# Kernel optimization log

Hardware: AMD Instinct MI355X
Metric: run time of the kernel (lower is better)

## Reference

```python
import jax, jax.numpy as jnp
import numpy as np

K_NEIGHBOURS = 4  # neighbour_num
BN_EPS = 1e-5


def setup_inputs() -> dict:
    key = jax.random.key(0)
    ks = jax.random.split(key, 5)
    B, T, J, C = 32, 243, 17, 256
    std = np.sqrt(2.0 / C).astype(np.float32)
    return {
        "x": jax.random.normal(ks[0], (B, T, J, C), dtype=jnp.float32),
        "W_u": jax.random.normal(ks[1], (C, C), dtype=jnp.float32) * std,
        "b_u": jnp.zeros((C,), dtype=jnp.float32),
        "W_v": jax.random.normal(ks[2], (C, C), dtype=jnp.float32) * std,
        "b_v": jnp.zeros((C,), dtype=jnp.float32),
        "gamma": jnp.ones((T,), dtype=jnp.float32),
        "beta": jnp.zeros((T,), dtype=jnp.float32),
    }


def reference(x, W_u, b_u, W_v, b_v, gamma, beta):
    # temporal-mode GCN with top-k similarity adjacency
    b, t, j, c = x.shape
    xr = jnp.transpose(x, (0, 2, 1, 3)).reshape(b * j, t, c)  # [BJ, T, C]

    # similarity adjacency: keep edges >= k-th largest similarity per row
    sim = jnp.einsum('bnc,bmc->bnm', xr, xr)                  # [BJ, T, T]
    thr = jax.lax.top_k(sim, K_NEIGHBOURS)[0][..., -1:]       # [BJ, T, 1]
    adj = (sim >= thr).astype(x.dtype)

    # symmetric degree normalization D^{-1/2} A D^{-1/2}
    deg_inv_sqrt = adj.sum(-1) ** -0.5                        # [BJ, T]
    norm_adj = deg_inv_sqrt[:, :, None] * adj * deg_inv_sqrt[:, None, :]

    v = xr @ W_v.T + b_v
    u = xr @ W_u.T + b_u
    h = jnp.einsum('bnm,bmc->bnc', norm_adj, v) + u           # [BJ, T, C]

    # BatchNorm1d(num_features=T), training mode: stats over (batch, C)
    mean = h.mean(axis=(0, 2), keepdims=True)
    var = jnp.mean((h - mean) ** 2, axis=(0, 2), keepdims=True)
    hn = (h - mean) * jax.lax.rsqrt(var + BN_EPS) * gamma[None, :, None] + beta[None, :, None]

    out = jax.nn.relu(xr + hn)                                # residual (dim_in == dim_out)
    return jnp.transpose(out.reshape(b, j, t, c), (0, 2, 1, 3))  # [B, T, J, C]
```

## Files before the change

kernel.cpp:

```cpp
#include <hip/hip_runtime.h>

#define BB 32
#define TT 243
#define JJ 17
#define CC 256
#define BJC (BB*JJ)
#define MM (BJC*TT)
#define FR (BJC*256)
#define SIMP 244
#define NEG_INF (-3.0e38f)

typedef __attribute__((ext_vector_type(8))) short bf16x8;
typedef __attribute__((ext_vector_type(4))) float f32x4;
typedef __attribute__((ext_vector_type(8))) _Float16 f16x8;
typedef __attribute__((ext_vector_type(4))) _Float16 f16x4;

__device__ __forceinline__ unsigned short f2bf(float f) {
  unsigned int u = __float_as_uint(f);
  u = (u + 0x7fffu + ((u >> 16) & 1u)) >> 16;
  return (unsigned short)u;
}
__device__ __forceinline__ float bf2f(unsigned short s) {
  return __uint_as_float(((unsigned int)s) << 16);
}

__device__ __forceinline__ void gld16(const void* g, void* l) {
  __builtin_amdgcn_global_load_lds(
      (__attribute__((address_space(1))) void*)(g),
      (__attribute__((address_space(3))) void*)(l), 16, 0, 0);
}

__launch_bounds__(256)
__global__ void k_prep_w(const float* __restrict__ Wu, const float* __restrict__ Wv,
                         _Float16* __restrict__ wcp) {
  const int r = blockIdx.x * 4 + (threadIdx.x >> 6);
  const int l = threadIdx.x & 63;
  const float* src = ((r < CC) ? (Wu + (size_t)r * CC) : (Wv + (size_t)(r - CC) * CC)) + l * 4;
  float4 v = *reinterpret_cast<const float4*>(src);
  f16x4 hv = (f16x4){(_Float16)v.x, (_Float16)v.y, (_Float16)v.z, (_Float16)v.w};
  const int ks = l >> 4;
  const int u  = (l & 15) >> 1;
  const int s  = u ^ (r & 7);
  *reinterpret_cast<f16x4*>(wcp + ((size_t)ks * 512 + r) * 64 + s * 8 + (l & 1) * 4) = hv;
}

__launch_bounds__(256)
__global__ void k_prep_x(const float* __restrict__ x,
                         _Float16* __restrict__ xqh, _Float16* __restrict__ xql) {
  const int r = blockIdx.x * 4 + (threadIdx.x >> 6);
  const int l = threadIdx.x & 63;
  const int bj = r / TT, t = r - bj * TT;
  const int b = bj / JJ, j = bj - b * JJ;
  float4 v = *reinterpret_cast<const float4*>(
      x + ((size_t)(b * TT + t) * JJ + j) * CC + l * 4);
  _Float16 h0 = (_Float16)v.x, h1 = (_Float16)v.y, h2 = (_Float16)v.z, h3 = (_Float16)v.w;
  f16x4 hv = (f16x4){h0, h1, h2, h3};
  f16x4 lv = (f16x4){(_Float16)(v.x - (float)h0), (_Float16)(v.y - (float)h1),
                     (_Float16)(v.z - (float)h2), (_Float16)(v.w - (float)h3)};
  const int fr = bj * 256 + t;
  const int ks = l >> 4;
  const int u  = (l & 15) >> 1;
  const int s  = u ^ (t & 7);
  const size_t off = ((size_t)ks * FR + fr) * 64 + s * 8 + (l & 1) * 4;
  *reinterpret_cast<f16x4*>(xqh + off) = hv;
  *reinterpret_cast<f16x4*>(xql + off) = lv;
}

__launch_bounds__(512, 4)
__global__ void k_sim(const _Float16* __restrict__ xqh, const _Float16* __restrict__ xql,
                      float* __restrict__ sim) {
  __shared__ _Float16 Sh[256 * 64];
  __shared__ _Float16 Sl[256 * 64];
  const int bid = blockIdx.x;
  const int g = bid >> 4, s_ = bid & 15;
  const int bj = g * 8 + (s_ & 7);
  const int rh = s_ >> 3;
  const int tid = threadIdx.x, lane = tid & 63, wid = tid >> 6;
  const int wr = wid >> 2, wc = wid & 3;
  const int rowbase = rh * 128 + wr * 64;
  const int l15 = lane & 15, lg = lane >> 4;
  const size_t rb = (size_t)bj * 256;
  const size_t lsrc = (size_t)(lane >> 3) * 64 + (lane & 7) * 8;

  f32x4 acc[4][4];
  #pragma unroll
  for (int i = 0; i < 4; i++)
    #pragma unroll
    for (int j = 0; j < 4; j++) acc[i][j] = (f32x4){0.f, 0.f, 0.f, 0.f};

  for (int ks = 0; ks < 4; ++ks) {
    {
      const _Float16* ph = xqh + ((size_t)ks * FR + rb) * 64;
      const _Float16* pl = xql + ((size_t)ks * FR + rb) * 64;
      #pragma unroll
      for (int c = 0; c < 4; ++c) {
        const int row0 = (wid * 4 + c) * 8;
        gld16(ph + (size_t)row0 * 64 + lsrc, &Sh[row0 * 64]);
        gld16(pl + (size_t)row0 * 64 + lsrc, &Sl[row0 * 64]);
      }
    }
    __syncthreads();
    #pragma unroll
    for (int kh = 0; kh < 2; ++kh) {
      f16x8 bhv[4], blv[4];
      #pragma unroll
      for (int j = 0; j < 4; ++j) {
        int rc = wc * 64 + j * 16 + l15;
        int sl = ((kh * 4 + lg) ^ (rc & 7)) * 8;
        bhv[j] = *reinterpret_cast<const f16x8*>(&Sh[rc * 64 + sl]);
        blv[j] = *reinterpret_cast<const f16x8*>(&Sl[rc * 64 + sl]);
      }
      #pragma unroll
      for (int i = 0; i < 4; ++i) {
        int rl = rowbase + i * 16 + l15;
        int sl = ((kh * 4 + lg) ^ (rl & 7)) * 8;
        f16x8 ah = *reinterpret_cast<const f16x8*>(&Sh[rl * 64 + sl]);
        f16x8 al = *reinterpret_cast<const f16x8*>(&Sl[rl * 64 + sl]);
        #pragma unroll
        for (int j = 0; j < 4; ++j) {
          acc[i][j] = __builtin_amdgcn_mfma_f32_16x16x32_f16(ah, bhv[j], acc[i][j], 0, 0, 0);
          acc[i][j] = __builtin_amdgcn_mfma_f32_16x16x32_f16(ah, blv[j], acc[i][j], 0, 0, 0);
          acc[i][j] = __builtin_amdgcn_mfma_f32_16x16x32_f16(al, bhv[j], acc[i][j], 0, 0, 0);
        }
      }
    }
    if (ks < 3) __syncthreads();
  }

  const size_t sbase = (size_t)bj * TT * SIMP;
  #pragma unroll
  for (int i = 0; i < 4; ++i) {
    #pragma unroll
    for (int q = 0; q < 4; ++q) {
      int n = rowbase + i * 16 + lg * 4 + q;
      if (n < TT) {
        #pragma unroll
        for (int j = 0; j < 4; ++j) {
          int c = wc * 64 + j * 16 + l15;
          if (c < TT) sim[sbase + (size_t)n * SIMP + c] = acc[i][j][q];
        }
      }
    }
  }
}

__launch_bounds__(256)
__global__ void k_uv(const _Float16* __restrict__ xqh, const _Float16* __restrict__ wcp,
                     const float* __restrict__ bu, const float* __restrict__ bv,
                     unsigned short* __restrict__ uo, unsigned short* __restrict__ vo) {
  __shared__ _Float16 S[2][128][64];
  const int ct = blockIdx.x;
  const int m0 = blockIdx.y * 128;
  const int tid = threadIdx.x, lane = tid & 63, wid = tid >> 6;
  const int rm = wid * 32;
  const int l15 = lane & 15, lg = lane >> 4;

  const float* bsrc = (ct < 2) ? bu : bv;
  unsigned short* osrc = (ct < 2) ? uo : vo;
  const int cb = (ct & 1) * 128;

  float bias[8];
  #pragma unroll
  for (int j = 0; j < 8; ++j) bias[j] = bsrc[cb + j * 16 + l15];

  f32x4 acc[2][8];
  #pragma unroll
  for (int i = 0; i < 2; i++)
    #pragma unroll
    for (int j = 0; j < 8; j++) acc[i][j] = (f32x4){0.f, 0.f, 0.f, 0.f};

  for (int ks = 0; ks < 4; ++ks) {
    #pragma unroll
    for (int c = 0; c < 8; ++c) {
      int ch = wid * 8 + c;
      int half = ch >> 4;
      int rows0 = (ch & 15) * 8;
      const _Float16* g = half
        ? wcp + ((size_t)ks * 512 + ct * 128 + rows0) * 64 + lane * 8
        : xqh + ((size_t)ks * FR  + m0       + rows0) * 64 + lane * 8;
      gld16(g, &S[half][rows0][0]);
    }
    __syncthreads();
    #pragma unroll
    for (int kh = 0; kh < 2; ++kh) {
      f16x8 af[2], bfv[8];
      #pragma unroll
      for (int i = 0; i < 2; ++i) {
        int rl = rm + i * 16 + l15;
        af[i] = *reinterpret_cast<const f16x8*>(&S[0][rl][((kh * 4 + lg) ^ (rl & 7)) * 8]);
      }
      #pragma unroll
      for (int j = 0; j < 8; ++j) {
        int rl = j * 16 + l15;
        bfv[j] = *reinterpret_cast<const f16x8*>(&S[1][rl][((kh * 4 + lg) ^ (rl & 7)) * 8]);
      }
      #pragma unroll
      for (int i = 0; i < 2; ++i)
        #pragma unroll
        for (int j = 0; j < 8; ++j)
          acc[i][j] = __builtin_amdgcn_mfma_f32_16x16x32_f16(af[i], bfv[j], acc[i][j], 0, 0, 0);
    }
    __syncthreads();
  }

  #pragma unroll
  for (int i = 0; i < 2; ++i) {
    #pragma unroll
    for (int q = 0; q < 4; ++q) {
      int gf = m0 + rm + i * 16 + lg * 4 + q;
      int t = gf & 255, bj = gf >> 8;
      if (t < TT) {
        size_t gm = (size_t)bj * TT + t;
        #pragma unroll
        for (int j = 0; j < 8; ++j)
          osrc[gm * CC + cb + j * 16 + l15] = f2bf(acc[i][j][q] + bias[j]);
      }
    }
  }
}

__launch_bounds__(256)
__global__ void k_topk(const float* __restrict__ sim,
                       float* __restrict__ dis_o,
                       unsigned long long* __restrict__ mask_o,
                       unsigned char* __restrict__ nbr_o,
                       unsigned char* __restrict__ deg_o) {
  const int l = threadIdx.x & 63, wv = threadIdx.x >> 6;
  const int r = blockIdx.x * 4 + wv;
  const float* row = sim + (size_t)r * SIMP;
  float o0 = row[l];
  float o1 = row[l + 64];
  float o2 = row[l + 128];
  float o3 = (l + 192 < TT) ? row[l + 192] : NEG_INF;
  float v0 = o0, v1 = o1, v2 = o2, v3 = o3;
  { float mx, mn;
    mx=fmaxf(v0,v1); mn=fminf(v0,v1); v0=mx; v1=mn;
    mx=fmaxf(v2,v3); mn=fminf(v2,v3); v2=mx; v3=mn;
    mx=fmaxf(v0,v2); mn=fminf(v0,v2); v0=mx; v2=mn;
    mx=fmaxf(v1,v3); mn=fminf(v1,v3); v1=mx; v3=mn;
    mx=fmaxf(v1,v2); mn=fminf(v1,v2); v1=mx; v2=mn; }
  #pragma unroll
  for (int off = 1; off < 64; off <<= 1) {
    float b0 = __shfl_xor(v0, off), b1 = __shfl_xor(v1, off),
          b2 = __shfl_xor(v2, off), b3 = __shfl_xor(v3, off);
    float t0 = fmaxf(v0, b3), t1 = fmaxf(v1, b2),
          t2 = fmaxf(v2, b1), t3 = fmaxf(v3, b0);
    float mx, mn;
    mx=fmaxf(t0,t2); mn=fminf(t0,t2); t0=mx; t2=mn;
    mx=fmaxf(t1,t3); mn=fminf(t1,t3); t1=mx; t3=mn;
    mx=fmaxf(t0,t1); mn=fminf(t0,t1); t0=mx; t1=mn;
    mx=fmaxf(t2,t3); mn=fminf(t2,t3); t2=mx; t3=mn;
    v0=t0; v1=t1; v2=t2; v3=t3;
  }
  const float thr = v3;

  unsigned long long m0 = __ballot(o0 >= thr);
  unsigned long long m1 = __ballot(o1 >= thr);
  unsigned long long m2 = __ballot(o2 >= thr);
  unsigned long long m3 = __ballot(o3 >= thr);
  const unsigned long long below = (1ull << l) - 1ull;
  const int b0 = __popcll(m0);
  const int b1 = b0 + __popcll(m1);
  const int b2 = b1 + __popcll(m2);
  const size_t r8 = (size_t)r * 8;
  if (o0 >= thr) { int q = __popcll(m0 & below);      if (q < 8) nbr_o[r8 + q] = (unsigned char)l; }
  if (o1 >= thr) { int q = b0 + __popcll(m1 & below); if (q < 8) nbr_o[r8 + q] = (unsigned char)(64 + l); }
  if (o2 >= thr) { int q = b1 + __popcll(m2 & below); if (q < 8) nbr_o[r8 + q] = (unsigned char)(128 + l); }
  if (o3 >= thr) { int q = b2 + __popcll(m3 & below); if (q < 8) nbr_o[r8 + q] = (unsigned char)(192 + l); }
  if (l == 0) {
    int deg = b2 + __popcll(m3);
    dis_o[r] = rsqrtf((float)deg);
    deg_o[r] = (unsigned char)((deg > 255) ? 255 : deg);
    mask_o[(size_t)r * 4 + 0] = m0;
    mask_o[(size_t)r * 4 + 1] = m1;
    mask_o[(size_t)r * 4 + 2] = m2;
    mask_o[(size_t)r * 4 + 3] = m3;
  }
}

__launch_bounds__(512)
__global__ void k_agg(const unsigned char* __restrict__ nbr,
                      const unsigned char* __restrict__ degv,
                      const unsigned long long* __restrict__ mask,
                      const float* __restrict__ dis,
                      const unsigned short* __restrict__ u,
                      const unsigned short* __restrict__ v,
                      unsigned short* __restrict__ h,
                      float* __restrict__ p1, float* __restrict__ p2) {
  __shared__ float dis_l[256];
  const int bj = blockIdx.x;
  const int tid = threadIdx.x, lane = tid & 63, wid = tid >> 6;
  if (tid < TT) dis_l[tid] = dis[(size_t)bj * TT + tid];
  __syncthreads();
  const int start = blockIdx.y * 122;
  const int cnt = blockIdx.y ? (TT - 122) : 122;
  const size_t pbase = (size_t)bj * TT;
  const int co = lane * 4;
  for (int rl = wid; rl < cnt; rl += 8) {
    const int t = start + rl;
    const size_t r = pbase + t;
    const float dr = dis_l[t];
    const int dg = degv[r];
    const unsigned long long nb = *reinterpret_cast<const unsigned long long*>(nbr + r * 8);
    ushort4 uu = *reinterpret_cast<const ushort4*>(u + r * CC + co);
    float a0 = bf2f(uu.x), a1 = bf2f(uu.y), a2 = bf2f(uu.z), a3 = bf2f(uu.w);
    if (dg <= 8) {
      const int i0 = (int)(nb & 255), i1 = (int)((nb >> 8) & 255),
                i2 = (int)((nb >> 16) & 255), i3 = (int)((nb >> 24) & 255);
      ushort4 w0v = *reinterpret_cast<const ushort4*>(v + (pbase + i0) * CC + co);
      ushort4 w1v = *reinterpret_cast<const ushort4*>(v + (pbase + i1) * CC + co);
      ushort4 w2v = *reinterpret_cast<const ushort4*>(v + (pbase + i2) * CC + co);
      ushort4 w3v = *reinterpret_cast<const ushort4*>(v + (pbase + i3) * CC + co);
      const float w0 = dr * dis_l[i0], w1 = dr * dis_l[i1],
                  w2 = dr * dis_l[i2], w3 = dr * dis_l[i3];
      a0 = __builtin_fmaf(w0, bf2f(w0v.x), a0); a1 = __builtin_fmaf(w0, bf2f(w0v.y), a1);
      a2 = __builtin_fmaf(w0, bf2f(w0v.z), a2); a3 = __builtin_fmaf(w0, bf2f(w0v.w), a3);
      a0 = __builtin_fmaf(w1, bf2f(w1v.x), a0); a1 = __builtin_fmaf(w1, bf2f(w1v.y), a1);
      a2 = __builtin_fmaf(w1, bf2f(w1v.z), a2); a3 = __builtin_fmaf(w1, bf2f(w1v.w), a3);
      a0 = __builtin_fmaf(w2, bf2f(w2v.x), a0); a1 = __builtin_fmaf(w2, bf2f(w2v.y), a1);
      a2 = __builtin_fmaf(w2, bf2f(w2v.z), a2); a3 = __builtin_fmaf(w2, bf2f(w2v.w), a3);
      a0 = __builtin_fmaf(w3, bf2f(w3v.x), a0); a1 = __builtin_fmaf(w3, bf2f(w3v.y), a1);
      a2 = __builtin_fmaf(w3, bf2f(w3v.z), a2); a3 = __builtin_fmaf(w3, bf2f(w3v.w), a3);
      #pragma unroll
      for (int e = 4; e < 8; ++e) {
        if (e < dg) {
          const int ix = (int)((nb >> (8 * e)) & 255);
          const float we = dr * dis_l[ix];
          ushort4 vv = *reinterpret_cast<const ushort4*>(v + (pbase + ix) * CC + co);
          a0 = __builtin_fmaf(we, bf2f(vv.x), a0); a1 = __builtin_fmaf(we, bf2f(vv.y), a1);
          a2 = __builtin_fmaf(we, bf2f(vv.z), a2); a3 = __builtin_fmaf(we, bf2f(vv.w), a3);
        }
      }
    } else {
      #pragma unroll
      for (int w4 = 0; w4 < 4; ++w4) {
        unsigned long long m = mask[r * 4 + w4];
        while (m) {
          int i = __ffsll(m) - 1;
          m &= m - 1;
          int idx = w4 * 64 + i;
          float w = dr * dis_l[idx];
          ushort4 vv = *reinterpret_cast<const ushort4*>(v + (pbase + idx) * CC + co);
          a0 = __builtin_fmaf(w, bf2f(vv.x), a0);
          a1 = __builtin_fmaf(w, bf2f(vv.y), a1);
          a2 = __builtin_fmaf(w, bf2f(vv.z), a2);
          a3 = __builtin_fmaf(w, bf2f(vv.w), a3);
        }
      }
    }
    ushort4 hh;
    hh.x = f2bf(a0); hh.y = f2bf(a1); hh.z = f2bf(a2); hh.w = f2bf(a3);
    *reinterpret_cast<ushort4*>(h + r * CC + co) = hh;
    float s1 = a0 + a1 + a2 + a3;
    float s2 = a0*a0 + a1*a1 + a2*a2 + a3*a3;
    #pragma unroll
    for (int off = 1; off < 64; off <<= 1) { s1 += __shfl_xor(s1, off); s2 += __shfl_xor(s2, off); }
    if (lane == 0) { p1[r] = s1; p2[r] = s2; }
  }
}

__global__ void k_bnstat(const float* __restrict__ p1, const float* __restrict__ p2,
                         const float* __restrict__ gamma, const float* __restrict__ beta,
                         float* __restrict__ scale, float* __restrict__ shift) {
  __shared__ float sA[256], sB[256];
  const int t = blockIdx.x;
  const int tid = threadIdx.x;
  float a = 0.f, b2 = 0.f;
  for (int bj = tid; bj < BJC; bj += 256) {
    a  += p1[bj * TT + t];
    b2 += p2[bj * TT + t];
  }
  sA[tid] = a; sB[tid] = b2;
  __syncthreads();
  for (int s = 128; s > 0; s >>= 1) {
    if (tid < s) { sA[tid] += sA[tid + s]; sB[tid] += sB[tid + s]; }
    __syncthreads();
  }
  if (tid == 0) {
    const float invN = 1.0f / (float)(BJC * CC);
    float mean = sA[0] * invN;
    float var  = sB[0] * invN - mean * mean;
    float sc   = rsqrtf(var + 1e-5f) * gamma[t];
    scale[t] = sc;
    shift[t] = beta[t] - mean * sc;
  }
}

__global__ void k_out(const float* __restrict__ x, const unsigned short* __restrict__ h,
                      const float* __restrict__ scale, const float* __restrict__ shift,
                      float* __restrict__ out) {
  int g = blockIdx.x * 256 + threadIdx.x;
  if (g >= MM * (CC/4)) return;
  int c4  = g & 63;
  int rowx = g >> 6;
  int b   = rowx / (TT*JJ);
  int rem = rowx - b*(TT*JJ);
  int t   = rem / JJ;
  int j   = rem - t*JJ;
  size_t hoff = ((size_t)(b*JJ + j) * TT + t) * CC + c4*4;
  float4 xv = *reinterpret_cast<const float4*>(x + (size_t)rowx*CC + c4*4);
  ushort4 hv = *reinterpret_cast<const ushort4*>(h + hoff);
  float sc = scale[t], sh = shift[t];
  float4 o;
  o.x = fmaxf(xv.x + bf2f(hv.x)*sc + sh, 0.f);
  o.y = fmaxf(xv.y + bf2f(hv.y)*sc + sh, 0.f);
  o.z = fmaxf(xv.z + bf2f(hv.z)*sc + sh, 0.f);
  o.w = fmaxf(xv.w + bf2f(hv.w)*sc + sh, 0.f);
  *reinterpret_cast<float4*>(out + (size_t)rowx*CC + c4*4) = o;
}

extern "C" void kernel_launch(void* const* d_in, const int* in_sizes, int n_in,
                              void* d_out, int out_size, void* d_ws, size_t ws_size,
                              hipStream_t stream) {
  const float* x     = (const float*)d_in[0];
  const float* Wu    = (const float*)d_in[1];
  const float* bu    = (const float*)d_in[2];
  const float* Wv    = (const float*)d_in[3];
  const float* bv    = (const float*)d_in[4];
  const float* gamma = (const float*)d_in[5];
  const float* beta  = (const float*)d_in[6];
  float* out = (float*)d_out;

  char* ws = (char*)d_ws;
  size_t off = 0;
  auto alloc = [&](size_t bytes) -> void* {
    void* p = ws + off;
    off = (off + bytes + 255) & ~(size_t)255;
    return p;
  };
  _Float16* xqh = (_Float16*)alloc((size_t)4 * FR * 64 * 2);
  _Float16* xql = (_Float16*)alloc((size_t)4 * FR * 64 * 2);
  _Float16* wcp = (_Float16*)alloc((size_t)4 * 512 * 64 * 2);
  float* sim = (float*)alloc((size_t)BJC * TT * SIMP * 4);
  float* dis = (float*)alloc((size_t)MM * 4);
  unsigned long long* msk = (unsigned long long*)alloc((size_t)MM * 4 * 8);
  unsigned char* nbr = (unsigned char*)alloc((size_t)MM * 8);
  unsigned char* deg = (unsigned char*)alloc((size_t)MM);
  float* p1    = (float*)alloc((size_t)MM * 4);
  float* p2    = (float*)alloc((size_t)MM * 4);
  float* scale = (float*)alloc(1024);
  float* shift = (float*)alloc(1024);
  unsigned short* v = (unsigned short*)alloc((size_t)MM * CC * 2);
  unsigned short* u = (unsigned short*)sim;
  unsigned short* h = (unsigned short*)xql;

  if (ws_size < off) {
    hipMemsetAsync(d_out, 0, (size_t)out_size * 4, stream);
    return;
  }

  k_prep_w<<<dim3(512/4), dim3(256), 0, stream>>>(Wu, Wv, wcp);
  k_prep_x<<<dim3(MM/4), dim3(256), 0, stream>>>(x, xqh, xql);
  k_sim  <<<dim3(BJC*2), dim3(512), 0, stream>>>(xqh, xql, sim);
  k_topk <<<dim3(MM/4), dim3(256), 0, stream>>>(sim, dis, msk, nbr, deg);
  k_uv   <<<dim3(4, FR/128), dim3(256), 0, stream>>>(xqh, wcp, bu, bv, u, v);
  k_agg  <<<dim3(BJC, 2), dim3(512), 0, stream>>>(nbr, deg, msk, dis, u, v, h, p1, p2);
  k_bnstat<<<dim3(TT), dim3(256), 0, stream>>>(p1, p2, gamma, beta, scale, shift);
  k_out  <<<dim3((MM*(CC/4) + 255)/256), dim3(256), 0, stream>>>(x, h, scale, shift, out);
}
```

Before: 385.5 us.

## Fuse top-k threshold selection into similarity GEMM epilogue, drop sim buffer

```diff
diff --git a/kernel.cpp b/kernel.cpp
--- a/kernel.cpp
+++ b/kernel.cpp
@@ -7,7 +7,6 @@
 #define BJC (BB*JJ)
 #define MM (BJC*TT)
 #define FR (BJC*256)
-#define SIMP 244
 #define NEG_INF (-3.0e38f)
 
 typedef __attribute__((ext_vector_type(8))) short bf16x8;
@@ -68,9 +67,13 @@
 
 __launch_bounds__(512, 4)
 __global__ void k_sim(const _Float16* __restrict__ xqh, const _Float16* __restrict__ xql,
-                      float* __restrict__ sim) {
-  __shared__ _Float16 Sh[256 * 64];
-  __shared__ _Float16 Sl[256 * 64];
+                      float* __restrict__ dis_o,
+                      unsigned long long* __restrict__ mask_o,
+                      unsigned char* __restrict__ nbr_o,
+                      unsigned char* __restrict__ deg_o) {
+  __shared__ __align__(16) char LB[65536];
+  _Float16* Sh = (_Float16*)LB;
+  _Float16* Sl = (_Float16*)(LB + 32768);
   const int bid = blockIdx.x;
   const int g = bid >> 4, s_ = bid & 15;
   const int bj = g * 8 + (s_ & 7);
@@ -95,8 +98,8 @@
       #pragma unroll
       for (int c = 0; c < 4; ++c) {
         const int row0 = (wid * 4 + c) * 8;
-        gld16(ph + (size_t)row0 * 64 + lsrc, &Sh[row0 * 64]);
-        gld16(pl + (size_t)row0 * 64 + lsrc, &Sl[row0 * 64]);
+        gld16(ph + (size_t)row0 * 64 + lsrc, Sh + row0 * 64);
+        gld16(pl + (size_t)row0 * 64 + lsrc, Sl + row0 * 64);
       }
     }
     __syncthreads();
@@ -124,22 +127,118 @@
         }
       }
     }
-    if (ks < 3) __syncthreads();
-  }
-
-  const size_t sbase = (size_t)bj * TT * SIMP;
+    __syncthreads();
+  }
+
+  float* top4 = (float*)LB;
+  unsigned long long* mlds = (unsigned long long*)(LB + 8192);
+  float* thrl = (float*)(LB + 8192 + 4096);
+
+  auto mval = [&](int i, int j, int q) -> float {
+    float x = acc[i][j][q];
+    if (wc == 3 && j == 3 && l15 >= 3) x = NEG_INF;
+    return x;
+  };
+
   #pragma unroll
   for (int i = 0; i < 4; ++i) {
     #pragma unroll
     for (int q = 0; q < 4; ++q) {
-      int n = rowbase + i * 16 + lg * 4 + q;
-      if (n < TT) {
+      float v0 = mval(i, 0, q), v1 = mval(i, 1, q),
+            v2 = mval(i, 2, q), v3 = mval(i, 3, q);
+      { float mx, mn;
+        mx=fmaxf(v0,v1); mn=fminf(v0,v1); v0=mx; v1=mn;
+        mx=fmaxf(v2,v3); mn=fminf(v2,v3); v2=mx; v3=mn;
+        mx=fmaxf(v0,v2); mn=fminf(v0,v2); v0=mx; v2=mn;
+        mx=fmaxf(v1,v3); mn=fminf(v1,v3); v1=mx; v3=mn;
+        mx=fmaxf(v1,v2); mn=fminf(v1,v2); v1=mx; v2=mn; }
+      #pragma unroll
+      for (int off = 1; off < 16; off <<= 1) {
+        float b0 = __shfl_xor(v0, off), b1 = __shfl_xor(v1, off),
+              b2 = __shfl_xor(v2, off), b3 = __shfl_xor(v3, off);
+        float t0 = fmaxf(v0, b3), t1 = fmaxf(v1, b2),
+              t2 = fmaxf(v2, b1), t3 = fmaxf(v3, b0);
+        float mx, mn;
+        mx=fmaxf(t0,t2); mn=fminf(t0,t2); t0=mx; t2=mn;
+        mx=fmaxf(t1,t3); mn=fminf(t1,t3); t1=mx; t3=mn;
+        mx=fmaxf(t0,t1); mn=fminf(t0,t1); t0=mx; t1=mn;
+        mx=fmaxf(t2,t3); mn=fminf(t2,t3); t2=mx; t3=mn;
+        v0=t0; v1=t1; v2=t2; v3=t3;
+      }
+      if (l15 == 0) {
+        int rloc = wr * 64 + i * 16 + lg * 4 + q;
+        float* d = &top4[(rloc * 4 + wc) * 4];
+        d[0] = v0; d[1] = v1; d[2] = v2; d[3] = v3;
+      }
+    }
+  }
+  __syncthreads();
+
+  if (tid < 128) {
+    float t0 = NEG_INF, t1 = NEG_INF, t2 = NEG_INF, t3 = NEG_INF;
+    #pragma unroll
+    for (int w = 0; w < 4; ++w) {
+      #pragma unroll
+      for (int e = 0; e < 4; ++e) {
+        float xv = top4[(tid * 4 + w) * 4 + e];
+        if (xv > t3) {
+          if (xv > t0)      { t3 = t2; t2 = t1; t1 = t0; t0 = xv; }
+          else if (xv > t1) { t3 = t2; t2 = t1; t1 = xv; }
+          else if (xv > t2) { t3 = t2; t2 = xv; }
+          else              { t3 = xv; }
+        }
+      }
+    }
+    thrl[tid] = t3;
+  }
+  __syncthreads();
+
+  #pragma unroll
+  for (int i = 0; i < 4; ++i) {
+    #pragma unroll
+    for (int q = 0; q < 4; ++q) {
+      const int rloc = wr * 64 + i * 16 + lg * 4 + q;
+      const float th = thrl[rloc];
+      unsigned long long bal[4];
+      #pragma unroll
+      for (int j = 0; j < 4; ++j) bal[j] = __ballot(mval(i, j, q) >= th);
+      if (l15 == 0) {
+        unsigned long long m = 0;
         #pragma unroll
-        for (int j = 0; j < 4; ++j) {
-          int c = wc * 64 + j * 16 + l15;
-          if (c < TT) sim[sbase + (size_t)n * SIMP + c] = acc[i][j][q];
+        for (int j = 0; j < 4; ++j)
+          m |= ((bal[j] >> (lg * 16)) & 0xFFFFull) << (j * 16);
+        mlds[rloc * 4 + wc] = m;
+      }
+    }
+  }
+  __syncthreads();
+
+  if (tid < 128) {
+    const int rn = rh * 128 + tid;
+    if (rn < TT) {
+      const size_t r = (size_t)bj * TT + rn;
+      unsigned long long m0 = mlds[tid * 4 + 0], m1 = mlds[tid * 4 + 1],
+                         m2 = mlds[tid * 4 + 2], m3 = mlds[tid * 4 + 3];
+      int deg = __popcll(m0) + __popcll(m1) + __popcll(m2) + __popcll(m3);
+      dis_o[r] = rsqrtf((float)deg);
+      deg_o[r] = (unsigned char)((deg > 255) ? 255 : deg);
+      mask_o[r * 4 + 0] = m0;
+      mask_o[r * 4 + 1] = m1;
+      mask_o[r * 4 + 2] = m2;
+      mask_o[r * 4 + 3] = m3;
+      unsigned long long nbv = 0;
+      int cnt = 0;
+      #pragma unroll
+      for (int w4 = 0; w4 < 4; ++w4) {
+        unsigned long long m = (w4 == 0) ? m0 : (w4 == 1) ? m1 : (w4 == 2) ? m2 : m3;
+        while (m && cnt < 8) {
+          int b = __ffsll(m) - 1;
+          m &= m - 1;
+          nbv |= ((unsigned long long)(w4 * 64 + b)) << (8 * cnt);
+          ++cnt;
         }
       }
+      *reinterpret_cast<unsigned long long*>(nbr_o + r * 8) = nbv;
     }
   }
 }
@@ -216,65 +315,6 @@
           osrc[gm * CC + cb + j * 16 + l15] = f2bf(acc[i][j][q] + bias[j]);
       }
     }
-  }
-}
-
-__launch_bounds__(256)
-__global__ void k_topk(const float* __restrict__ sim,
-                       float* __restrict__ dis_o,
-                       unsigned long long* __restrict__ mask_o,
-                       unsigned char* __restrict__ nbr_o,
-                       unsigned char* __restrict__ deg_o) {
-  const int l = threadIdx.x & 63, wv = threadIdx.x >> 6;
-  const int r = blockIdx.x * 4 + wv;
-  const float* row = sim + (size_t)r * SIMP;
-  float o0 = row[l];
-  float o1 = row[l + 64];
-  float o2 = row[l + 128];
-  float o3 = (l + 192 < TT) ? row[l + 192] : NEG_INF;
-  float v0 = o0, v1 = o1, v2 = o2, v3 = o3;
-  { float mx, mn;
-    mx=fmaxf(v0,v1); mn=fminf(v0,v1); v0=mx; v1=mn;
-    mx=fmaxf(v2,v3); mn=fminf(v2,v3); v2=mx; v3=mn;
-    mx=fmaxf(v0,v2); mn=fminf(v0,v2); v0=mx; v2=mn;
-    mx=fmaxf(v1,v3); mn=fminf(v1,v3); v1=mx; v3=mn;
-    mx=fmaxf(v1,v2); mn=fminf(v1,v2); v1=mx; v2=mn; }
-  #pragma unroll
-  for (int off = 1; off < 64; off <<= 1) {
-    float b0 = __shfl_xor(v0, off), b1 = __shfl_xor(v1, off),
-          b2 = __shfl_xor(v2, off), b3 = __shfl_xor(v3, off);
-    float t0 = fmaxf(v0, b3), t1 = fmaxf(v1, b2),
-          t2 = fmaxf(v2, b1), t3 = fmaxf(v3, b0);
-    float mx, mn;
-    mx=fmaxf(t0,t2); mn=fminf(t0,t2); t0=mx; t2=mn;
-    mx=fmaxf(t1,t3); mn=fminf(t1,t3); t1=mx; t3=mn;
-    mx=fmaxf(t0,t1); mn=fminf(t0,t1); t0=mx; t1=mn;
-    mx=fmaxf(t2,t3); mn=fminf(t2,t3); t2=mx; t3=mn;
-    v0=t0; v1=t1; v2=t2; v3=t3;
-  }
-  const float thr = v3;
-
-  unsigned long long m0 = __ballot(o0 >= thr);
-  unsigned long long m1 = __ballot(o1 >= thr);
-  unsigned long long m2 = __ballot(o2 >= thr);
-  unsigned long long m3 = __ballot(o3 >= thr);
-  const unsigned long long below = (1ull << l) - 1ull;
-  const int b0 = __popcll(m0);
-  const int b1 = b0 + __popcll(m1);
-  const int b2 = b1 + __popcll(m2);
-  const size_t r8 = (size_t)r * 8;
-  if (o0 >= thr) { int q = __popcll(m0 & below);      if (q < 8) nbr_o[r8 + q] = (unsigned char)l; }
-  if (o1 >= thr) { int q = b0 + __popcll(m1 & below); if (q < 8) nbr_o[r8 + q] = (unsigned char)(64 + l); }
-  if (o2 >= thr) { int q = b1 + __popcll(m2 & below); if (q < 8) nbr_o[r8 + q] = (unsigned char)(128 + l); }
-  if (o3 >= thr) { int q = b2 + __popcll(m3 & below); if (q < 8) nbr_o[r8 + q] = (unsigned char)(192 + l); }
-  if (l == 0) {
-    int deg = b2 + __popcll(m3);
-    dis_o[r] = rsqrtf((float)deg);
-    deg_o[r] = (unsigned char)((deg > 255) ? 255 : deg);
-    mask_o[(size_t)r * 4 + 0] = m0;
-    mask_o[(size_t)r * 4 + 1] = m1;
-    mask_o[(size_t)r * 4 + 2] = m2;
-    mask_o[(size_t)r * 4 + 3] = m3;
   }
 }
 
@@ -431,7 +471,6 @@
   _Float16* xqh = (_Float16*)alloc((size_t)4 * FR * 64 * 2);
   _Float16* xql = (_Float16*)alloc((size_t)4 * FR * 64 * 2);
   _Float16* wcp = (_Float16*)alloc((size_t)4 * 512 * 64 * 2);
-  float* sim = (float*)alloc((size_t)BJC * TT * SIMP * 4);
   float* dis = (float*)alloc((size_t)MM * 4);
   unsigned long long* msk = (unsigned long long*)alloc((size_t)MM * 4 * 8);
   unsigned char* nbr = (unsigned char*)alloc((size_t)MM * 8);
@@ -440,8 +479,8 @@
   float* p2    = (float*)alloc((size_t)MM * 4);
   float* scale = (float*)alloc(1024);
   float* shift = (float*)alloc(1024);
+  unsigned short* u = (unsigned short*)alloc((size_t)MM * CC * 2);
   unsigned short* v = (unsigned short*)alloc((size_t)MM * CC * 2);
-  unsigned short* u = (unsigned short*)sim;
   unsigned short* h = (unsigned short*)xql;
 
   if (ws_size < off) {
@@ -451,8 +490,7 @@
 
   k_prep_w<<<dim3(512/4), dim3(256), 0, stream>>>(Wu, Wv, wcp);
   k_prep_x<<<dim3(MM/4), dim3(256), 0, stream>>>(x, xqh, xql);
-  k_sim  <<<dim3(BJC*2), dim3(512), 0, stream>>>(xqh, xql, sim);
-  k_topk <<<dim3(MM/4), dim3(256), 0, stream>>>(sim, dis, msk, nbr, deg);
+  k_sim  <<<dim3(BJC*2), dim3(512), 0, stream>>>(xqh, xql, dis, msk, nbr, deg);
   k_uv   <<<dim3(4, FR/128), dim3(256), 0, stream>>>(xqh, wcp, bu, bv, u, v);
   k_agg  <<<dim3(BJC, 2), dim3(512), 0, stream>>>(nbr, deg, msk, dis, u, v, h, p1, p2);
   k_bnstat<<<dim3(TT), dim3(256), 0, stream>>>(p1, p2, gamma, beta, scale, shift);
```

New measurement: 338.2 us. 12.3% less time.
